# Performance work log

Hardware: AMD Instinct MI355X
Metric: run time of the kernel (lower is better)

## Reference

```python
import jax, jax.numpy as jnp
import numpy as np

N_EMBD = 1024
N_HEAD = 16
HEAD_DIM = N_EMBD // N_HEAD


def setup_inputs() -> dict:
    key = jax.random.key(0)
    k1, k2, k3 = jax.random.split(key, 3)
    x = jax.random.normal(k1, (4, 2048, N_EMBD), dtype=jnp.float32)
    w_qkv = jax.random.normal(k2, (N_EMBD, 3 * N_EMBD), dtype=jnp.float32) * (N_EMBD ** -0.5)
    w_proj = jax.random.normal(k3, (N_EMBD, N_EMBD), dtype=jnp.float32) * (N_EMBD ** -0.5)
    return {"x": x, "w_qkv": w_qkv, "w_proj": w_proj}


def reference(x, w_qkv, w_proj):
    B, T, C = x.shape
    qkv = jnp.einsum('btc,cd->btd', x, w_qkv)  # [B,T,3C]
    q, k, v = jnp.split(qkv, 3, axis=-1)
    def heads(t):
        return t.reshape(B, T, N_HEAD, HEAD_DIM).transpose(0, 2, 1, 3)  # [B,H,T,D]
    q, k, v = heads(q), heads(k), heads(v)
    scale = 1.0 / jnp.sqrt(jnp.asarray(HEAD_DIM, dtype=x.dtype))
    att = jnp.einsum('bhqd,bhkd->bhqk', q, k) * scale  # [B,H,T,T]
    causal = jnp.tril(jnp.ones((T, T), dtype=bool))
    att = jnp.where(causal[None, None], att, jnp.asarray(-jnp.inf, dtype=att.dtype))
    att = jax.nn.softmax(att, axis=-1)
    out = jnp.einsum('bhqk,bhkd->bhqd', att, v)  # [B,H,T,D]
    out = out.transpose(0, 2, 1, 3).reshape(B, T, C)
    return jnp.einsum('btc,cd->btd', out, w_proj)
```

## Files before the change

### kernel.cpp

```cpp
#include <hip/hip_runtime.h>
#include <cstdint>
#include <cstddef>
#include <type_traits>

typedef float  f32x4    __attribute__((ext_vector_type(4)));
typedef float  f32x16   __attribute__((ext_vector_type(16)));
typedef __bf16 bf16x8   __attribute__((ext_vector_type(8)));
typedef short  short4_t __attribute__((ext_vector_type(4)));
typedef short  short8_t __attribute__((ext_vector_type(8)));
typedef unsigned int uint4_t __attribute__((ext_vector_type(4)));

__device__ __forceinline__ short f2bf(float f) {
  return __builtin_bit_cast(short, (__bf16)f);
}

__device__ __forceinline__ unsigned pk2bf(float a, float b) {
  unsigned lo = (unsigned short)__builtin_bit_cast(unsigned short, f2bf(a));
  unsigned hi = (unsigned short)__builtin_bit_cast(unsigned short, f2bf(b));
  return lo | (hi << 16);
}

__device__ __forceinline__ void gl_lds16(const void* g, void* l) {
  __builtin_amdgcn_global_load_lds((const __attribute__((address_space(1))) void*)g,
                                   (__attribute__((address_space(3))) void*)l, 16, 0, 0);
}

__global__ void convert_bf16(const float* __restrict__ X, short* __restrict__ Xb) {
  int i = (blockIdx.x * 256 + threadIdx.x) * 4;
  f32x4 v = *(const f32x4*)&X[i];
  short4_t o;
#pragma unroll
  for (int j = 0; j < 4; j++) o[j] = f2bf(v[j]);
  *(short4_t*)&Xb[i] = o;
}

__global__ void transpose_bf16(const float* __restrict__ W, short* __restrict__ WT,
                               int K, int N) {
  __shared__ float tile[32][33];
  int tx = threadIdx.x & 31, ty = threadIdx.x >> 5;
  int n0 = blockIdx.x * 32, k0 = blockIdx.y * 32;
#pragma unroll
  for (int i = 0; i < 32; i += 8)
    tile[ty + i][tx] = W[(size_t)(k0 + ty + i) * N + n0 + tx];
  __syncthreads();
#pragma unroll
  for (int i = 0; i < 32; i += 8)
    WT[(size_t)(n0 + ty + i) * K + k0 + tx] = f2bf(tile[tx][ty + i]);
}

template <int MODE>
__global__ __launch_bounds__(256, 2) void gemm_bt(
    const short* __restrict__ A, const short* __restrict__ Bt,
    float* __restrict__ outf, short* __restrict__ Qo, short* __restrict__ Ko,
    short* __restrict__ Vo, int M, int N, int K) {
  __shared__ alignas(16) short As[128 * 32];
  __shared__ alignas(16) short Bs[128 * 32];
  const int tid = threadIdx.x;
  const int lane = tid & 63;
  const int g = lane & 15, q = lane >> 4;
  const int wave = tid >> 6;
  const int m0 = blockIdx.y * 128, n0 = blockIdx.x * 128;
  const int wm = (wave >> 1) * 64, wn = (wave & 1) * 64;

  const int srow = tid >> 2;
  const int scol = (tid & 3) * 8;
  const short* ap0 = A  + (size_t)(m0 + srow) * K + scol;
  const short* ap1 = A  + (size_t)(m0 + 64 + srow) * K + scol;
  const short* bp0 = Bt + (size_t)(n0 + srow) * K + scol;
  const short* bp1 = Bt + (size_t)(n0 + 64 + srow) * K + scol;
  short* la0 = &As[tid * 8];
  short* la1 = &As[(tid + 256) * 8];
  short* lb0 = &Bs[tid * 8];
  short* lb1 = &Bs[(tid + 256) * 8];

  f32x4 acc[4][4] = {};

  for (int k0 = 0; k0 < K; k0 += 32) {
    __syncthreads();
    gl_lds16(ap0 + k0, la0);
    gl_lds16(ap1 + k0, la1);
    gl_lds16(bp0 + k0, lb0);
    gl_lds16(bp1 + k0, lb1);
    __syncthreads();
    bf16x8 af[4], bfr[4];
#pragma unroll
    for (int mt = 0; mt < 4; mt++)
      af[mt] = *(const bf16x8*)&As[(wm + mt * 16 + g) * 32 + q * 8];
#pragma unroll
    for (int nt = 0; nt < 4; nt++)
      bfr[nt] = *(const bf16x8*)&Bs[(wn + nt * 16 + g) * 32 + q * 8];
#pragma unroll
    for (int mt = 0; mt < 4; mt++)
#pragma unroll
      for (int nt = 0; nt < 4; nt++)
        acc[mt][nt] = __builtin_amdgcn_mfma_f32_16x16x32_bf16(af[mt], bfr[nt],
                                                              acc[mt][nt], 0, 0, 0);
  }

  if (MODE == 0) {
#pragma unroll
    for (int mt = 0; mt < 4; mt++)
#pragma unroll
      for (int nt = 0; nt < 4; nt++) {
        int n = n0 + wn + nt * 16 + g;
        int mbase = m0 + wm + mt * 16 + q * 4;
#pragma unroll
        for (int r = 0; r < 4; r++)
          outf[(size_t)(mbase + r) * N + n] = acc[mt][nt][r];
      }
  } else {
#pragma unroll
    for (int nt = 0; nt < 4; nt++) {
      int n = n0 + wn + nt * 16 + g;
      int which = n >> 10;
      int c = n & 1023;
      int h = c >> 6, d = c & 63;
#pragma unroll
      for (int mt = 0; mt < 4; mt++) {
        int mbase = m0 + wm + mt * 16 + q * 4;
        int b = mbase >> 11, t = mbase & 2047;
        if (which == 2) {
          short4_t pv;
#pragma unroll
          for (int r = 0; r < 4; r++) pv[r] = f2bf(acc[mt][nt][r]);
          *(short4_t*)&Vo[((size_t)((b << 4) + h) * 64 + d) * 2048 + t] = pv;
        } else {
          short* dst = (which == 0) ? Qo : Ko;
#pragma unroll
          for (int r = 0; r < 4; r++)
            dst[((size_t)((b << 4) + h) * 2048 + (t + r)) * 64 + d] =
                f2bf(acc[mt][nt][r]);
        }
      }
    }
  }
}

__global__ __launch_bounds__(256, 2) void attn_fwd(
    const short* __restrict__ Qg, const short* __restrict__ Kg,
    const short* __restrict__ Vt, short* __restrict__ Og) {
  __shared__ alignas(16) short Ks[2][8192];
  __shared__ alignas(16) short Vs[2][8192];
  const int tid = threadIdx.x, lane = tid & 63, wave = tid >> 6;
  const int c = lane & 31;
  const int qh = lane >> 5;
  const int bh = blockIdx.x;
  const int b = bh >> 4, h = bh & 15;
  const size_t base = (size_t)bh * (2048 * 64);
  const float cs = 0.18033688011f;
  const int q_rel = wave * 32 + c;
  const int laneoff = (qh * 32 + c) * 8;

  const short* kp[4];
  const short* vp[4];
#pragma unroll
  for (int i = 0; i < 4; i++) {
    int u = i * 256 + tid;
    int uc = u & 31, uq = (u >> 5) & 1;
    kp[i] = Kg + base + (size_t)((u >> 8) * 32 + uc) * 64 + ((u >> 6) & 3) * 16 + uq * 8;
    vp[i] = Vt + base + (size_t)(((u >> 6) & 1) * 32 + uc) * 2048 + (u >> 7) * 16 + uq * 8;
  }

  auto stage = [&](int buf, int kt) {
    short* kd = &Ks[buf][tid * 8];
    short* vd = &Vs[buf][tid * 8];
#pragma unroll
    for (int i = 0; i < 4; i++) {
      gl_lds16(kp[i] + (size_t)kt * (128 * 64), kd + i * 2048);
      gl_lds16(vp[i] + (size_t)kt * 128, vd + i * 2048);
    }
  };

  int cur = 0;

  for (int half = 0; half < 2; half++) {
    const int qt = (half == 0) ? (int)blockIdx.y : 15 - (int)blockIdx.y;
    const int qrow = qt * 128 + wave * 32 + c;

    bf16x8 bq[4];
#pragma unroll
    for (int ks = 0; ks < 4; ks++) {
      bf16x8 v = *(const bf16x8*)&Qg[base + (size_t)qrow * 64 + ks * 16 + qh * 8];
#pragma unroll
      for (int j = 0; j < 8; j++) v[j] = (__bf16)((float)v[j] * cs);
      bq[ks] = v;
    }

    f32x16 ot[2] = {};
    float m_run = -1e30f, l_run = 0.0f;

    auto step = [&](auto diagc, const short* ksb, const short* vsb) {
      constexpr bool DIAG = decltype(diagc)::value;

      f32x16 st[4] = {};
      __builtin_amdgcn_s_setprio(1);
#pragma unroll
      for (int mt = 0; mt < 4; mt++)
#pragma unroll
        for (int ks = 0; ks < 4; ks++) {
          bf16x8 ak = *(const bf16x8*)&ksb[(mt * 4 + ks) * 512 + laneoff];
          st[mt] = __builtin_amdgcn_mfma_f32_32x32x16_bf16(ak, bq[ks],
                                                           st[mt], 0, 0, 0);
        }
      __builtin_amdgcn_s_setprio(0);

      float tm[4];
#pragma unroll
      for (int mt = 0; mt < 4; mt++) {
        float t = -1e30f;
#pragma unroll
        for (int r = 0; r < 16; r++) {
          if (DIAG) {
            int krel = mt * 32 + (r & 3) + 8 * (r >> 2) + 4 * qh;
            if (krel > q_rel) st[mt][r] = -1e30f;
          }
          t = fmaxf(t, st[mt][r]);
        }
        tm[mt] = t;
      }
      float tmax = fmaxf(fmaxf(tm[0], tm[1]), fmaxf(tm[2], tm[3]));
      tmax = fmaxf(tmax, __shfl_xor(tmax, 32));
      if (!__all(tmax - m_run <= 8.0f)) {
        const float mnew = fmaxf(m_run, tmax);
        const float alpha = __builtin_amdgcn_exp2f(m_run - mnew);
        l_run *= alpha;
#pragma unroll
        for (int mt = 0; mt < 2; mt++)
#pragma unroll
          for (int r = 0; r < 16; r++) ot[mt][r] *= alpha;
        m_run = mnew;
      }
      float ps[4];
#pragma unroll
      for (int mt = 0; mt < 4; mt++) {
        float s = 0.0f;
#pragma unroll
        for (int r = 0; r < 16; r++) {
          float p = __builtin_amdgcn_exp2f(st[mt][r] - m_run);
          s += p;
          st[mt][r] = p;
        }
        ps[mt] = s;
      }
      float psum = (ps[0] + ps[1]) + (ps[2] + ps[3]);
      psum += __shfl_xor(psum, 32);
      l_run += psum;

      __builtin_amdgcn_s_setprio(1);
#pragma unroll
      for (int kb = 0; kb < 8; kb++) {
        const int mt = kb >> 1, rb = (kb & 1) * 8;
        unsigned x0 = pk2bf(st[mt][rb + 0], st[mt][rb + 1]);
        unsigned x1 = pk2bf(st[mt][rb + 2], st[mt][rb + 3]);
        unsigned y0 = pk2bf(st[mt][rb + 4], st[mt][rb + 5]);
        unsigned y1 = pk2bf(st[mt][rb + 6], st[mt][rb + 7]);
        asm("v_permlane32_swap_b32 %0, %1" : "+v"(x0), "+v"(y0));
        asm("v_permlane32_swap_b32 %0, %1" : "+v"(x1), "+v"(y1));
        uint4_t pw;
        pw[0] = x0; pw[1] = x1; pw[2] = y0; pw[3] = y1;
        bf16x8 pb = __builtin_bit_cast(bf16x8, pw);
#pragma unroll
        for (int mtv = 0; mtv < 2; mtv++) {
          bf16x8 av = *(const bf16x8*)&vsb[(kb * 2 + mtv) * 512 + laneoff];
          ot[mtv] = __builtin_amdgcn_mfma_f32_32x32x16_bf16(av, pb,
                                                            ot[mtv], 0, 0, 0);
        }
      }
      __builtin_amdgcn_s_setprio(0);
    };

    __syncthreads();
    stage(cur, 0);
    for (int kt = 0; kt <= qt; kt++) {
      __syncthreads();
      if (kt < qt) stage(cur ^ 1, kt + 1);
      if (kt == qt)
        step(std::integral_constant<bool, true>{}, Ks[cur], Vs[cur]);
      else
        step(std::integral_constant<bool, false>{}, Ks[cur], Vs[cur]);
      cur ^= 1;
    }

    const float inv = 1.0f / l_run;
    const size_t obase = ((size_t)b * 2048 + qrow) * 1024 + h * 64 + qh * 4;
#pragma unroll
    for (int mt = 0; mt < 2; mt++)
#pragma unroll
      for (int rr = 0; rr < 4; rr++) {
        short4_t ov;
#pragma unroll
        for (int i = 0; i < 4; i++) ov[i] = f2bf(ot[mt][rr * 4 + i] * inv);
        *(short4_t*)&Og[obase + mt * 32 + rr * 8] = ov;
      }
  }
}

extern "C" void kernel_launch(void* const* d_in, const int* in_sizes, int n_in,
                              void* d_out, int out_size, void* d_ws, size_t ws_size,
                              hipStream_t stream) {
  const float* x      = (const float*)d_in[0];
  const float* w_qkv  = (const float*)d_in[1];
  const float* w_proj = (const float*)d_in[2];
  float* out = (float*)d_out;

  char* ws = (char*)d_ws;
  short* xb     = (short*)(ws);
  short* wqkvT  = (short*)(ws + 16777216);
  short* wprojT = (short*)(ws + 23068672);
  short* Qb     = (short*)(ws + 25165824);
  short* Kb     = (short*)(ws + 41943040);
  short* Vtb    = (short*)(ws + 58720256);

  convert_bf16<<<8192, 256, 0, stream>>>(x, xb);
  {
    dim3 gq(96, 32); transpose_bf16<<<gq, 256, 0, stream>>>(w_qkv, wqkvT, 1024, 3072);
    dim3 gp(32, 32); transpose_bf16<<<gp, 256, 0, stream>>>(w_proj, wprojT, 1024, 1024);
  }
  {
    dim3 g(24, 64);
    gemm_bt<1><<<g, 256, 0, stream>>>(xb, wqkvT, nullptr, Qb, Kb, Vtb, 8192, 3072, 1024);
  }
  {
    dim3 g(64, 8);
    attn_fwd<<<g, 256, 0, stream>>>(Qb, Kb, Vtb, xb );
  }
  {
    dim3 g(8, 64);
    gemm_bt<0><<<g, 256, 0, stream>>>(xb, wprojT, out, nullptr, nullptr, nullptr,
                                      8192, 1024, 1024);
  }
}
```

Baseline: 254.3 us.

## Share K/V tile loads between paired query tiles and fuse prep kernels

The attention kernel now processes its low and high query tiles together in one pass over the key/value tiles. Each staged K/V tile is reused by both query tiles, where before the low tile's keys were loaded twice, and one load/sync pipeline replaces two. Separately, the input conversion and the two weight transposes are merged into a single prep launch to cut launch overhead. The cost is higher register pressure from holding two sets of Q fragments and accumulators, which could lower occupancy or cause spills.

```diff
diff --git a/kernel.cpp b/kernel.cpp
--- a/kernel.cpp
+++ b/kernel.cpp
@@ -25,20 +25,29 @@
                                    (__attribute__((address_space(3))) void*)l, 16, 0, 0);
 }
 
-__global__ void convert_bf16(const float* __restrict__ X, short* __restrict__ Xb) {
-  int i = (blockIdx.x * 256 + threadIdx.x) * 4;
-  f32x4 v = *(const f32x4*)&X[i];
-  short4_t o;
-#pragma unroll
-  for (int j = 0; j < 4; j++) o[j] = f2bf(v[j]);
-  *(short4_t*)&Xb[i] = o;
-}
-
-__global__ void transpose_bf16(const float* __restrict__ W, short* __restrict__ WT,
-                               int K, int N) {
+__global__ void prep(const float* __restrict__ x, short* __restrict__ xb,
+                     const float* __restrict__ wqkv, short* __restrict__ wqkvT,
+                     const float* __restrict__ wproj, short* __restrict__ wprojT) {
   __shared__ float tile[32][33];
-  int tx = threadIdx.x & 31, ty = threadIdx.x >> 5;
-  int n0 = blockIdx.x * 32, k0 = blockIdx.y * 32;
+  const int bid = blockIdx.x, tid = threadIdx.x;
+  if (bid < 8192) {
+    int i = (bid * 256 + tid) * 4;
+    f32x4 v = *(const f32x4*)&x[i];
+    short4_t o;
+#pragma unroll
+    for (int j = 0; j < 4; j++) o[j] = f2bf(v[j]);
+    *(short4_t*)&xb[i] = o;
+    return;
+  }
+  const float* W; short* WT; int N, bx, by;
+  if (bid < 11264) {
+    int r = bid - 8192;  W = wqkv;  WT = wqkvT;  N = 3072; bx = r % 96; by = r / 96;
+  } else {
+    int r = bid - 11264; W = wproj; WT = wprojT; N = 1024; bx = r % 32; by = r / 32;
+  }
+  const int K = 1024;
+  int tx = tid & 31, ty = tid >> 5;
+  int n0 = bx * 32, k0 = by * 32;
 #pragma unroll
   for (int i = 0; i < 32; i += 8)
     tile[ty + i][tx] = W[(size_t)(k0 + ty + i) * N + n0 + tx];
@@ -171,117 +180,136 @@
     }
   };
 
+  const int qlo = blockIdx.y, qhi = 15 - qlo;
+
+  bf16x8 bqL[4], bqH[4];
+  {
+    const int qrL = qlo * 128 + wave * 32 + c;
+    const int qrH = qhi * 128 + wave * 32 + c;
+#pragma unroll
+    for (int ks = 0; ks < 4; ks++) {
+      bf16x8 vL = *(const bf16x8*)&Qg[base + (size_t)qrL * 64 + ks * 16 + qh * 8];
+      bf16x8 vH = *(const bf16x8*)&Qg[base + (size_t)qrH * 64 + ks * 16 + qh * 8];
+#pragma unroll
+      for (int j = 0; j < 8; j++) {
+        vL[j] = (__bf16)((float)vL[j] * cs);
+        vH[j] = (__bf16)((float)vH[j] * cs);
+      }
+      bqL[ks] = vL; bqH[ks] = vH;
+    }
+  }
+
+  f32x16 otL[2] = {}, otH[2] = {};
+  float mL = -1e30f, lL = 0.0f, mH = -1e30f, lH = 0.0f;
+
+  auto step = [&](auto diagc, auto hic, const short* ksb, const short* vsb) {
+    constexpr bool DIAG = decltype(diagc)::value;
+    constexpr bool HI = decltype(hic)::value;
+    bf16x8* bq   = HI ? bqH : bqL;
+    f32x16* ot   = HI ? otH : otL;
+    float& m_run = HI ? mH : mL;
+    float& l_run = HI ? lH : lL;
+
+    f32x16 st[4] = {};
+    __builtin_amdgcn_s_setprio(1);
+#pragma unroll
+    for (int mt = 0; mt < 4; mt++)
+#pragma unroll
+      for (int ks = 0; ks < 4; ks++) {
+        bf16x8 ak = *(const bf16x8*)&ksb[(mt * 4 + ks) * 512 + laneoff];
+        st[mt] = __builtin_amdgcn_mfma_f32_32x32x16_bf16(ak, bq[ks],
+                                                         st[mt], 0, 0, 0);
+      }
+    __builtin_amdgcn_s_setprio(0);
+
+    float tm[4];
+#pragma unroll
+    for (int mt = 0; mt < 4; mt++) {
+      float t = -1e30f;
+#pragma unroll
+      for (int r = 0; r < 16; r++) {
+        if (DIAG) {
+          int krel = mt * 32 + (r & 3) + 8 * (r >> 2) + 4 * qh;
+          if (krel > q_rel) st[mt][r] = -1e30f;
+        }
+        t = fmaxf(t, st[mt][r]);
+      }
+      tm[mt] = t;
+    }
+    float tmax = fmaxf(fmaxf(tm[0], tm[1]), fmaxf(tm[2], tm[3]));
+    tmax = fmaxf(tmax, __shfl_xor(tmax, 32));
+    if (!__all(tmax - m_run <= 8.0f)) {
+      const float mnew = fmaxf(m_run, tmax);
+      const float alpha = __builtin_amdgcn_exp2f(m_run - mnew);
+      l_run *= alpha;
+#pragma unroll
+      for (int mt = 0; mt < 2; mt++)
+#pragma unroll
+        for (int r = 0; r < 16; r++) ot[mt][r] *= alpha;
+      m_run = mnew;
+    }
+    float ps[4];
+#pragma unroll
+    for (int mt = 0; mt < 4; mt++) {
+      float s = 0.0f;
+#pragma unroll
+      for (int r = 0; r < 16; r++) {
+        float p = __builtin_amdgcn_exp2f(st[mt][r] - m_run);
+        s += p;
+        st[mt][r] = p;
+      }
+      ps[mt] = s;
+    }
+    float psum = (ps[0] + ps[1]) + (ps[2] + ps[3]);
+    psum += __shfl_xor(psum, 32);
+    l_run += psum;
+
+    __builtin_amdgcn_s_setprio(1);
+#pragma unroll
+    for (int kb = 0; kb < 8; kb++) {
+      const int mt = kb >> 1, rb = (kb & 1) * 8;
+      unsigned x0 = pk2bf(st[mt][rb + 0], st[mt][rb + 1]);
+      unsigned x1 = pk2bf(st[mt][rb + 2], st[mt][rb + 3]);
+      unsigned y0 = pk2bf(st[mt][rb + 4], st[mt][rb + 5]);
+      unsigned y1 = pk2bf(st[mt][rb + 6], st[mt][rb + 7]);
+      asm("v_permlane32_swap_b32 %0, %1" : "+v"(x0), "+v"(y0));
+      asm("v_permlane32_swap_b32 %0, %1" : "+v"(x1), "+v"(y1));
+      uint4_t pw;
+      pw[0] = x0; pw[1] = x1; pw[2] = y0; pw[3] = y1;
+      bf16x8 pb = __builtin_bit_cast(bf16x8, pw);
+#pragma unroll
+      for (int mtv = 0; mtv < 2; mtv++) {
+        bf16x8 av = *(const bf16x8*)&vsb[(kb * 2 + mtv) * 512 + laneoff];
+        ot[mtv] = __builtin_amdgcn_mfma_f32_32x32x16_bf16(av, pb,
+                                                          ot[mtv], 0, 0, 0);
+      }
+    }
+    __builtin_amdgcn_s_setprio(0);
+  };
+
+  constexpr std::integral_constant<bool, false> F{};
+  constexpr std::integral_constant<bool, true>  T{};
+
   int cur = 0;
-
-  for (int half = 0; half < 2; half++) {
-    const int qt = (half == 0) ? (int)blockIdx.y : 15 - (int)blockIdx.y;
+  stage(0, 0);
+  for (int kt = 0; kt <= qhi; kt++) {
+    __syncthreads();
+    if (kt < qhi) stage(cur ^ 1, kt + 1);
+    if (kt <= qlo) {
+      if (kt == qlo) step(T, F, Ks[cur], Vs[cur]);
+      else           step(F, F, Ks[cur], Vs[cur]);
+    }
+    if (kt == qhi) step(T, T, Ks[cur], Vs[cur]);
+    else           step(F, T, Ks[cur], Vs[cur]);
+    cur ^= 1;
+  }
+
+#pragma unroll
+  for (int ti = 0; ti < 2; ti++) {
+    const int qt = ti ? qhi : qlo;
+    const f32x16* ot = ti ? otH : otL;
+    const float inv = 1.0f / (ti ? lH : lL);
     const int qrow = qt * 128 + wave * 32 + c;
-
-    bf16x8 bq[4];
-#pragma unroll
-    for (int ks = 0; ks < 4; ks++) {
-      bf16x8 v = *(const bf16x8*)&Qg[base + (size_t)qrow * 64 + ks * 16 + qh * 8];
-#pragma unroll
-      for (int j = 0; j < 8; j++) v[j] = (__bf16)((float)v[j] * cs);
-      bq[ks] = v;
-    }
-
-    f32x16 ot[2] = {};
-    float m_run = -1e30f, l_run = 0.0f;
-
-    auto step = [&](auto diagc, const short* ksb, const short* vsb) {
-      constexpr bool DIAG = decltype(diagc)::value;
-
-      f32x16 st[4] = {};
-      __builtin_amdgcn_s_setprio(1);
-#pragma unroll
-      for (int mt = 0; mt < 4; mt++)
-#pragma unroll
-        for (int ks = 0; ks < 4; ks++) {
-          bf16x8 ak = *(const bf16x8*)&ksb[(mt * 4 + ks) * 512 + laneoff];
-          st[mt] = __builtin_amdgcn_mfma_f32_32x32x16_bf16(ak, bq[ks],
-                                                           st[mt], 0, 0, 0);
-        }
-      __builtin_amdgcn_s_setprio(0);
-
-      float tm[4];
-#pragma unroll
-      for (int mt = 0; mt < 4; mt++) {
-        float t = -1e30f;
-#pragma unroll
-        for (int r = 0; r < 16; r++) {
-          if (DIAG) {
-            int krel = mt * 32 + (r & 3) + 8 * (r >> 2) + 4 * qh;
-            if (krel > q_rel) st[mt][r] = -1e30f;
-          }
-          t = fmaxf(t, st[mt][r]);
-        }
-        tm[mt] = t;
-      }
-      float tmax = fmaxf(fmaxf(tm[0], tm[1]), fmaxf(tm[2], tm[3]));
-      tmax = fmaxf(tmax, __shfl_xor(tmax, 32));
-      if (!__all(tmax - m_run <= 8.0f)) {
-        const float mnew = fmaxf(m_run, tmax);
-        const float alpha = __builtin_amdgcn_exp2f(m_run - mnew);
-        l_run *= alpha;
-#pragma unroll
-        for (int mt = 0; mt < 2; mt++)
-#pragma unroll
-          for (int r = 0; r < 16; r++) ot[mt][r] *= alpha;
-        m_run = mnew;
-      }
-      float ps[4];
-#pragma unroll
-      for (int mt = 0; mt < 4; mt++) {
-        float s = 0.0f;
-#pragma unroll
-        for (int r = 0; r < 16; r++) {
-          float p = __builtin_amdgcn_exp2f(st[mt][r] - m_run);
-          s += p;
-          st[mt][r] = p;
-        }
-        ps[mt] = s;
-      }
-      float psum = (ps[0] + ps[1]) + (ps[2] + ps[3]);
-      psum += __shfl_xor(psum, 32);
-      l_run += psum;
-
-      __builtin_amdgcn_s_setprio(1);
-#pragma unroll
-      for (int kb = 0; kb < 8; kb++) {
-        const int mt = kb >> 1, rb = (kb & 1) * 8;
-        unsigned x0 = pk2bf(st[mt][rb + 0], st[mt][rb + 1]);
-        unsigned x1 = pk2bf(st[mt][rb + 2], st[mt][rb + 3]);
-        unsigned y0 = pk2bf(st[mt][rb + 4], st[mt][rb + 5]);
-        unsigned y1 = pk2bf(st[mt][rb + 6], st[mt][rb + 7]);
-        asm("v_permlane32_swap_b32 %0, %1" : "+v"(x0), "+v"(y0));
-        asm("v_permlane32_swap_b32 %0, %1" : "+v"(x1), "+v"(y1));
-        uint4_t pw;
-        pw[0] = x0; pw[1] = x1; pw[2] = y0; pw[3] = y1;
-        bf16x8 pb = __builtin_bit_cast(bf16x8, pw);
-#pragma unroll
-        for (int mtv = 0; mtv < 2; mtv++) {
-          bf16x8 av = *(const bf16x8*)&vsb[(kb * 2 + mtv) * 512 + laneoff];
-          ot[mtv] = __builtin_amdgcn_mfma_f32_32x32x16_bf16(av, pb,
-                                                            ot[mtv], 0, 0, 0);
-        }
-      }
-      __builtin_amdgcn_s_setprio(0);
-    };
-
-    __syncthreads();
-    stage(cur, 0);
-    for (int kt = 0; kt <= qt; kt++) {
-      __syncthreads();
-      if (kt < qt) stage(cur ^ 1, kt + 1);
-      if (kt == qt)
-        step(std::integral_constant<bool, true>{}, Ks[cur], Vs[cur]);
-      else
-        step(std::integral_constant<bool, false>{}, Ks[cur], Vs[cur]);
-      cur ^= 1;
-    }
-
-    const float inv = 1.0f / l_run;
     const size_t obase = ((size_t)b * 2048 + qrow) * 1024 + h * 64 + qh * 4;
 #pragma unroll
     for (int mt = 0; mt < 2; mt++)
@@ -311,11 +339,7 @@
   short* Kb     = (short*)(ws + 41943040);
   short* Vtb    = (short*)(ws + 58720256);
 
-  convert_bf16<<<8192, 256, 0, stream>>>(x, xb);
-  {
-    dim3 gq(96, 32); transpose_bf16<<<gq, 256, 0, stream>>>(w_qkv, wqkvT, 1024, 3072);
-    dim3 gp(32, 32); transpose_bf16<<<gp, 256, 0, stream>>>(w_proj, wprojT, 1024, 1024);
-  }
+  prep<<<12288, 256, 0, stream>>>(x, xb, w_qkv, wqkvT, w_proj, wprojT);
   {
     dim3 g(24, 64);
     gemm_bt<1><<<g, 256, 0, stream>>>(xb, wqkvT, nullptr, Qb, Kb, Vtb, 8192, 3072, 1024);
```

Result: no change. 257.0 us (+1.1%).
